# Kernel optimization log

Hardware: AMD Instinct MI355X
Metric: run time of the kernel (lower is better)

The kernel has to match this reference:

```python
import jax, jax.numpy as jnp
import numpy as np

N_NODES, IN_DIM, HID, N_CLS, N_T = 4096, 512, 256, 128, 20


def _odefunc(x, A, Wt, bt):
    # X' = relu(Linear(A @ X)); dropout=0.0 so it is the identity
    return jax.nn.relu((A @ x) @ Wt.T + bt)


def _rk4_traj(vt, x0, A, Wt, bt):
    # torchdiffeq 'rk4' = fixed-grid 3/8-rule RK4 stepping between consecutive vt points
    f = lambda y: _odefunc(y, A, Wt, bt)  # autonomous: t unused by ODEFunc

    def step(x, dt):
        k1 = f(x)
        k2 = f(x + dt * k1 / 3.0)
        k3 = f(x + dt * (k2 - k1 / 3.0))
        k4 = f(x + dt * (k1 - k2 + k3))
        xn = x + dt * (k1 + 3.0 * k2 + 3.0 * k3 + k4) / 8.0
        return xn, xn

    dts = vt[1:] - vt[:-1]
    _, ys = jax.lax.scan(step, x0, dts)
    return jnp.concatenate([x0[None], ys], axis=0)  # [T, N, H]


def setup_inputs() -> dict:
    key = jax.random.key(0)
    ks = jax.random.split(key, 8)
    vt = jnp.arange(N_T, dtype=jnp.float32) * 0.05  # increasing time ticks, horizon ~1.0
    x = jax.random.normal(ks[0], (N_NODES, IN_DIM), dtype=jnp.float32)
    # row-scaled dense adjacency (torch.mm dense path); spectral scale ~O(1)
    A = jax.random.uniform(ks[1], (N_NODES, N_NODES), dtype=jnp.float32) / N_NODES
    W1 = jax.random.normal(ks[2], (HID, IN_DIM), dtype=jnp.float32) / np.sqrt(IN_DIM)
    b1 = jnp.zeros((HID,), dtype=jnp.float32)
    W2 = jax.random.normal(ks[3], (HID, HID), dtype=jnp.float32) / np.sqrt(HID)
    b2 = jnp.zeros((HID,), dtype=jnp.float32)
    Wt = jax.random.normal(ks[4], (HID, HID), dtype=jnp.float32) * (0.5 / np.sqrt(HID))
    bt = jnp.zeros((HID,), dtype=jnp.float32)
    Wo = jax.random.normal(ks[5], (N_CLS, HID), dtype=jnp.float32) / np.sqrt(HID)
    bo = jnp.zeros((N_CLS,), dtype=jnp.float32)
    return {"vt": vt, "x": x, "A": A, "W1": W1, "b1": b1, "W2": W2,
            "b2": b2, "Wt": Wt, "bt": bt, "Wo": Wo, "bo": bo}


def reference(vt, x, A, W1, b1, W2, b2, Wt, bt, Wo, bo):
    # input_layer: Linear -> Tanh -> Linear (dropout = 0.0 elsewhere)
    h = jnp.tanh(x @ W1.T + b1) @ W2.T + b2            # [N, H]
    traj = _rk4_traj(vt, h, A, Wt, bt)                 # [T, N, H] (terminal=False -> full trajectory)
    return traj @ Wo.T + bo                            # [T, N, C]
```

## Files before the change

### kernel.cpp

```cpp
#include <hip/hip_runtime.h>
#include <stdint.h>

typedef __bf16 bf16;
typedef bf16 bf16x8 __attribute__((ext_vector_type(8)));
typedef float f32x4 __attribute__((ext_vector_type(4)));
typedef uint32_t u32;
typedef unsigned long long u64;
typedef unsigned char u8;

#define NN   4096
#define HID  256
#define NCLS 128

__device__ __forceinline__ void gload16(const void* g, void* l) {
  __builtin_amdgcn_global_load_lds((const __attribute__((address_space(1))) u32*)g,
                                   (__attribute__((address_space(3))) u32*)l, 16, 0, 0);
}

__global__ void convf2b(const float* __restrict__ s, bf16* __restrict__ d, int n) {
  int i = (blockIdx.x * blockDim.x + threadIdx.x) * 4;
  if (i >= n) return;
  f32x4 v = *(const f32x4*)(s + i);
  bf16 o[4] = {(bf16)v[0], (bf16)v[1], (bf16)v[2], (bf16)v[3]};
  *(u64*)(d + i) = *(u64*)o;
}

__global__ void convAf8(const float* __restrict__ s, u8* __restrict__ d, int n) {
  int i = (blockIdx.x * blockDim.x + threadIdx.x) * 4;
  if (i >= n) return;
  f32x4 v = *(const f32x4*)(s + i);
  u32 pk = __builtin_amdgcn_cvt_pk_fp8_f32(v[0] * 4096.f, v[1] * 4096.f, 0, false);
  pk = __builtin_amdgcn_cvt_pk_fp8_f32(v[2] * 4096.f, v[3] * 4096.f, pk, true);
  *(u32*)(d + i) = pk;
}

__device__ __forceinline__ f32x4 ksplit_reduce(char* smem, f32x4 acc[2][2],
                                               int kw, int sw, int hh, int rl) {
  float* fs = (float*)smem;
  #pragma unroll
  for (int q = 0; q < 4; ++q) {
    const int src = (kw < q) ? kw : kw - 1;
    float* dst = fs + ((q * 3 + src) * 2 + sw) * 272;
    const int mf = q >> 1, nf = q & 1;
    if (q != kw) {
      #pragma unroll
      for (int j = 0; j < 4; ++j) dst[(hh * 4 + j) * 17 + rl] = acc[mf][nf][j];
    }
  }
  asm volatile("s_waitcnt lgkmcnt(0)" ::: "memory");
  __builtin_amdgcn_s_barrier();
  f32x4 r;
  if (kw == 0)      r = acc[0][0];
  else if (kw == 1) r = acc[0][1];
  else if (kw == 2) r = acc[1][0];
  else              r = acc[1][1];
  #pragma unroll
  for (int src = 0; src < 3; ++src) {
    const float* sp = fs + ((kw * 3 + src) * 2 + sw) * 272;
    #pragma unroll
    for (int j = 0; j < 4; ++j) r[j] += sp[(hh * 4 + j) * 17 + rl];
  }
  return r;
}

__global__ __launch_bounds__(512, 2) void gemmf8(
    const u8* __restrict__ Ag,
    const u8* __restrict__ Bg,
    bf16* __restrict__ Cb)
{
  __shared__ __align__(16) char smem[73728];
  const int tid = threadIdx.x;
  const int l = tid & 63, wv = tid >> 6;
  const int kw = wv & 3, sw = wv >> 2;
  const int rl = l & 15, hh = l >> 4;

  const int chunk = gridDim.x >> 3;
  const int sb = (blockIdx.x & 7) * chunk + (blockIdx.x >> 3);
  const int m0 = (sb >> 3) * 64, n0 = (sb & 7) * 32;

  const bool isB = wv >= 4;
  const int w4 = wv & 3;
  const int rlo = l >> 4;
  const int gq = l & 15;
  const int rowbase = isB ? n0 + w4 * 8 : m0 + w4 * 16;
  const u8* sGbase = (isB ? Bg : Ag) + (size_t)rowbase * 4096;
  const int c0 = (gq ^ rlo) << 4;
  const int c1 = (gq ^ (rlo + 4)) << 4;
  const int stoff = isB ? 16384 + w4 * 2048 : w4 * 4096;

  f32x4 acc[2][2];
  #pragma unroll
  for (int i = 0; i < 2; ++i)
    #pragma unroll
    for (int j = 0; j < 2; ++j) acc[i][j] = (f32x4){0.f, 0.f, 0.f, 0.f};

  auto stage = [&](int buf, int t) {
    char* base = smem + buf * 24576 + stoff;
    const u8* g = sGbase + (size_t)rlo * 4096 + t * 256;
    gload16(g + c0,                      base);
    gload16(g + (size_t)4  * 4096 + c1,  base + 1024);
    if (!isB) {
      gload16(g + (size_t)8  * 4096 + c0, base + 2048);
      gload16(g + (size_t)12 * 4096 + c1, base + 3072);
    }
  };

  auto compute = [&](int buf) {
    const char* As = smem + buf * 24576;
    const char* Bs = As + 16384;
    #pragma unroll
    for (int ks = 0; ks < 2; ++ks) {
      const int g0 = (kw * 2 + ks) * 2 + (hh >> 1);
      const int co = ((g0 ^ (rl & 7)) << 4) + (hh & 1) * 8;
      u64 a0 = *(const u64*)(As + (sw * 32 + rl +  0) * 256 + co);
      u64 a1 = *(const u64*)(As + (sw * 32 + rl + 16) * 256 + co);
      u64 b0 = *(const u64*)(Bs + (rl +  0) * 256 + co);
      u64 b1 = *(const u64*)(Bs + (rl + 16) * 256 + co);
      __builtin_amdgcn_s_setprio(1);
      acc[0][0] = __builtin_amdgcn_mfma_f32_16x16x32_fp8_fp8((long)a0, (long)b0, acc[0][0], 0, 0, 0);
      acc[0][1] = __builtin_amdgcn_mfma_f32_16x16x32_fp8_fp8((long)a0, (long)b1, acc[0][1], 0, 0, 0);
      acc[1][0] = __builtin_amdgcn_mfma_f32_16x16x32_fp8_fp8((long)a1, (long)b0, acc[1][0], 0, 0, 0);
      acc[1][1] = __builtin_amdgcn_mfma_f32_16x16x32_fp8_fp8((long)a1, (long)b1, acc[1][1], 0, 0, 0);
      __builtin_amdgcn_s_setprio(0);
    }
  };

  stage(0, 0); stage(1, 1);
  int cur = 0, pre = 2;
  for (int t = 0; t < 16; ++t) {
    if (t < 15) {
      if (!isB) { asm volatile("s_waitcnt vmcnt(4)" ::: "memory"); }
      else      { asm volatile("s_waitcnt vmcnt(2)" ::: "memory"); }
    } else       { asm volatile("s_waitcnt vmcnt(0)" ::: "memory"); }
    __builtin_amdgcn_sched_barrier(0);
    __builtin_amdgcn_s_barrier();
    __builtin_amdgcn_sched_barrier(0);
    if (t + 2 < 16) stage(pre, t + 2);
    compute(cur);
    cur = (cur == 2) ? 0 : cur + 1;
    pre = (pre == 2) ? 0 : pre + 1;
  }
  __builtin_amdgcn_s_barrier();
  __builtin_amdgcn_sched_barrier(0);

  f32x4 o = ksplit_reduce(smem, acc, kw, sw, hh, rl);
  const int row0 = m0 + sw * 32 + (kw >> 1) * 16 + hh * 4;
  const int col  = n0 + (kw & 1) * 16 + rl;
  #pragma unroll
  for (int r = 0; r < 4; ++r)
    Cb[(row0 + r) * HID + col] = (bf16)(o[r] * 2.44140625e-4f);
}

template<int EPI, int KK>
__global__ __launch_bounds__(512, 2) void gemmbf(
    const bf16* __restrict__ Ag, int lda,
    const bf16* __restrict__ Bg, int ldb,
    int Ntiles,
    const float* __restrict__ bias,
    float* __restrict__ outf,
    bf16* __restrict__ outb,
    u8* __restrict__ ybt,
    float* __restrict__ xbuf,
    const float* __restrict__ kk1,
    const float* __restrict__ kk2,
    const float* __restrict__ kk3,
    const float* __restrict__ vt, int step)
{
  __shared__ __align__(16) char smem[49152];
  const int tid = threadIdx.x;
  const int l = tid & 63, wv = tid >> 6;
  const int kw = wv & 3, sw = wv >> 2;
  const int rl = l & 15, hh = l >> 4;

  const int chunk = gridDim.x >> 3;
  const int sb = (blockIdx.x & 7) * chunk + (blockIdx.x >> 3);
  const int mtile = sb / Ntiles;
  const int ntile = sb - mtile * Ntiles;
  const int m0 = mtile * 64, n0 = ntile * 32;

  const bool isB = wv >= 4;
  const int w4 = wv & 3;

  f32x4 acc[2][2];
  #pragma unroll
  for (int i = 0; i < 2; ++i)
    #pragma unroll
    for (int j = 0; j < 2; ++j) acc[i][j] = (f32x4){0.f, 0.f, 0.f, 0.f};

  if constexpr (KK == 256) {
    const int lrow = l >> 5, lg = l & 31;
    if (!isB) {
      const char* gb = (const char*)(Ag + (size_t)(m0 + w4 * 16) * lda);
      char* base = smem + w4 * 8192;
      #pragma unroll
      for (int i = 0; i < 8; ++i) {
        const int r = i * 2 + lrow;
        const int swz = (lg ^ ((w4 * 16 + r) & 7)) << 4;
        gload16(gb + (size_t)r * lda * 2 + swz, base + i * 1024);
      }
    } else {
      const char* gb = (const char*)(Bg + (size_t)(n0 + w4 * 8) * ldb);
      char* base = smem + 32768 + w4 * 4096;
      #pragma unroll
      for (int i = 0; i < 4; ++i) {
        const int r = i * 2 + lrow;
        const int swz = (lg ^ ((w4 * 8 + r) & 7)) << 4;
        gload16(gb + (size_t)r * ldb * 2 + swz, base + i * 1024);
      }
    }
    asm volatile("s_waitcnt vmcnt(0)" ::: "memory");
    __builtin_amdgcn_sched_barrier(0);
    __builtin_amdgcn_s_barrier();
    __builtin_amdgcn_sched_barrier(0);

    const char* As = smem;
    const char* Bs = smem + 32768;
    #pragma unroll
    for (int ks = 0; ks < 2; ++ks) {
      const int ca = ((((kw * 2 + ks) * 4 + hh) ^ (rl & 7)) << 4);
      bf16x8 a0 = *(const bf16x8*)(As + (sw * 32 + rl +  0) * 512 + ca);
      bf16x8 a1 = *(const bf16x8*)(As + (sw * 32 + rl + 16) * 512 + ca);
      bf16x8 b0 = *(const bf16x8*)(Bs + (rl +  0) * 512 + ca);
      bf16x8 b1 = *(const bf16x8*)(Bs + (rl + 16) * 512 + ca);
      __builtin_amdgcn_s_setprio(1);
      acc[0][0] = __builtin_amdgcn_mfma_f32_16x16x32_bf16(a0, b0, acc[0][0], 0, 0, 0);
      acc[0][1] = __builtin_amdgcn_mfma_f32_16x16x32_bf16(a0, b1, acc[0][1], 0, 0, 0);
      acc[1][0] = __builtin_amdgcn_mfma_f32_16x16x32_bf16(a1, b0, acc[1][0], 0, 0, 0);
      acc[1][1] = __builtin_amdgcn_mfma_f32_16x16x32_bf16(a1, b1, acc[1][1], 0, 0, 0);
      __builtin_amdgcn_s_setprio(0);
    }
    __builtin_amdgcn_s_barrier();
    __builtin_amdgcn_sched_barrier(0);
  } else {
    const int rlo = l >> 4, gq = l & 15;
    const size_t ldby = (size_t)(isB ? ldb : lda) * 2;
    const int grow = (isB ? n0 + w4 * 8 : m0 + w4 * 16) + rlo;
    const char* sGb = (const char*)(isB ? (const void*)Bg : (const void*)Ag)
                      + (size_t)grow * ldby;
    const int c0 = (gq ^ rlo) << 4;
    const int c1 = (gq ^ (rlo + 4)) << 4;
    const int stoff = isB ? 16384 + w4 * 2048 : w4 * 4096;

    auto stage = [&](int buf, int t) {
      char* base = smem + buf * 24576 + stoff;
      const char* g = sGb + (size_t)t * 256;
      gload16(g + c0,            base);
      gload16(g + 4 * ldby + c1, base + 1024);
      if (!isB) {
        gload16(g +  8 * ldby + c0, base + 2048);
        gload16(g + 12 * ldby + c1, base + 3072);
      }
    };

    const int ca = ((kw * 4 + hh) ^ (rl & 7)) << 4;
    auto compute = [&](int buf) {
      const char* As = smem + buf * 24576;
      const char* Bs = As + 16384;
      bf16x8 a0 = *(const bf16x8*)(As + (sw * 32 + rl +  0) * 256 + ca);
      bf16x8 a1 = *(const bf16x8*)(As + (sw * 32 + rl + 16) * 256 + ca);
      bf16x8 b0 = *(const bf16x8*)(Bs + (rl +  0) * 256 + ca);
      bf16x8 b1 = *(const bf16x8*)(Bs + (rl + 16) * 256 + ca);
      __builtin_amdgcn_s_setprio(1);
      acc[0][0] = __builtin_amdgcn_mfma_f32_16x16x32_bf16(a0, b0, acc[0][0], 0, 0, 0);
      acc[0][1] = __builtin_amdgcn_mfma_f32_16x16x32_bf16(a0, b1, acc[0][1], 0, 0, 0);
      acc[1][0] = __builtin_amdgcn_mfma_f32_16x16x32_bf16(a1, b0, acc[1][0], 0, 0, 0);
      acc[1][1] = __builtin_amdgcn_mfma_f32_16x16x32_bf16(a1, b1, acc[1][1], 0, 0, 0);
      __builtin_amdgcn_s_setprio(0);
    };

    const int nmac = KK >> 7;
    stage(0, 0);
    asm volatile("s_waitcnt vmcnt(0)" ::: "memory");
    __builtin_amdgcn_s_barrier();
    int cur = 0;
    for (int t = 0; t < nmac; ++t) {
      if (t + 1 < nmac) stage(cur ^ 1, t + 1);
      compute(cur);
      asm volatile("s_waitcnt vmcnt(0)" ::: "memory");
      __builtin_amdgcn_sched_barrier(0);
      __builtin_amdgcn_s_barrier();
      cur ^= 1;
    }
    __builtin_amdgcn_sched_barrier(0);
  }

  f32x4 o = ksplit_reduce(smem, acc, kw, sw, hh, rl);
  const int row0 = m0 + sw * 32 + (kw >> 1) * 16 + hh * 4;
  const int col  = n0 + (kw & 1) * 16 + rl;

  float dtv = 0.f;
  if constexpr (EPI >= 3 && EPI <= 6) dtv = vt[step + 1] - vt[step];

  if constexpr (EPI == 1) {
    #pragma unroll
    for (int r = 0; r < 4; ++r)
      outb[(row0 + r) * HID + col] = (bf16)tanhf(o[r] + bias[col]);
  } else if constexpr (EPI == 2) {
    float yv[4];
    #pragma unroll
    for (int r = 0; r < 4; ++r) {
      float v = o[r] + bias[col];
      xbuf[(row0 + r) * HID + col] = v;
      outb[(row0 + r) * HID + col] = (bf16)v;
      yv[r] = v;
    }
    u32 pk = __builtin_amdgcn_cvt_pk_fp8_f32(yv[0], yv[1], 0, false);
    pk = __builtin_amdgcn_cvt_pk_fp8_f32(yv[2], yv[3], pk, true);
    *(u32*)(ybt + (size_t)col * NN + row0) = pk;
  } else if constexpr (EPI >= 3 && EPI <= 6) {
    float yv[4];
    #pragma unroll
    for (int r = 0; r < 4; ++r) {
      const int idx = (row0 + r) * HID + col;
      float v = fmaxf(o[r] + bias[col], 0.f);
      float xv = xbuf[idx];
      float y;
      if constexpr (EPI == 3)      { outf[idx] = v; y = xv + dtv * (1.f/3.f) * v; }
      else if constexpr (EPI == 4) { outf[idx] = v; y = xv + dtv * (v - kk1[idx] * (1.f/3.f)); }
      else if constexpr (EPI == 5) { outf[idx] = v; y = xv + dtv * (kk1[idx] - kk2[idx] + v); }
      else {
        float xn = xv + dtv * 0.125f * (kk1[idx] + 3.f*kk2[idx] + 3.f*kk3[idx] + v);
        xbuf[idx] = xn;
        outb[idx] = (bf16)xn;
        y = xn;
      }
      yv[r] = y;
    }
    u32 pk = __builtin_amdgcn_cvt_pk_fp8_f32(yv[0], yv[1], 0, false);
    pk = __builtin_amdgcn_cvt_pk_fp8_f32(yv[2], yv[3], pk, true);
    *(u32*)(ybt + (size_t)col * NN + row0) = pk;
  } else {
    #pragma unroll
    for (int r = 0; r < 4; ++r)
      outf[(size_t)(row0 + r) * NCLS + col] = o[r] + bias[col];
  }
}

extern "C" void kernel_launch(void* const* d_in, const int* in_sizes, int n_in,
                              void* d_out, int out_size, void* d_ws, size_t ws_size,
                              hipStream_t stream)
{
  const float* vt = (const float*)d_in[0];
  const float* x  = (const float*)d_in[1];
  const float* A  = (const float*)d_in[2];
  const float* W1 = (const float*)d_in[3];
  const float* b1 = (const float*)d_in[4];
  const float* W2 = (const float*)d_in[5];
  const float* b2 = (const float*)d_in[6];
  const float* Wt = (const float*)d_in[7];
  const float* bt = (const float*)d_in[8];
  const float* Wo = (const float*)d_in[9];
  const float* bo = (const float*)d_in[10];
  float* out = (float*)d_out;

  char* p = (char*)d_ws;
  auto carve = [&](size_t n) { char* r = p; p += (n + 255) & ~(size_t)255; return r; };
  u8*   A8  = (u8*)carve((size_t)4096 * 4096);
  bf16* xb  = (bf16*)carve((size_t)4096 * 512 * 2);
  bf16* W1b = (bf16*)carve((size_t)256 * 512 * 2);
  bf16* W2b = (bf16*)carve((size_t)256 * 256 * 2);
  bf16* Wtb = (bf16*)carve((size_t)256 * 256 * 2);
  bf16* Wob = (bf16*)carve((size_t)128 * 256 * 2);
  bf16* T1b = (bf16*)carve((size_t)4096 * 256 * 2);
  bf16* Cb  = (bf16*)carve((size_t)4096 * 256 * 2);
  u8*   Y8  = (u8*)carve((size_t)256 * 4096);
  float* xs = (float*)carve((size_t)4096 * 256 * 4);
  float* k1 = (float*)carve((size_t)4096 * 256 * 4);
  float* k2 = (float*)carve((size_t)4096 * 256 * 4);
  float* k3 = (float*)carve((size_t)4096 * 256 * 4);
  size_t base_need = (size_t)(p - (char*)d_ws);
  const size_t trajBytes = (size_t)20 * 4096 * 256 * 2;
  bool big = (ws_size >= base_need + trajBytes);
  bf16* traj = (bf16*)carve(big ? trajBytes : (size_t)4096 * 256 * 2);

  convAf8<<<16384, 256, 0, stream>>>(A,  A8,  16777216);
  convf2b<<<2048,  256, 0, stream>>>(x,  xb,  2097152);
  convf2b<<<128,   256, 0, stream>>>(W1, W1b, 131072);
  convf2b<<<64,    256, 0, stream>>>(W2, W2b, 65536);
  convf2b<<<64,    256, 0, stream>>>(Wt, Wtb, 65536);
  convf2b<<<32,    256, 0, stream>>>(Wo, Wob, 32768);

  gemmbf<1, 512><<<512, 512, 0, stream>>>(xb, 512, W1b, 512, 8, b1,
      nullptr, T1b, nullptr, nullptr, nullptr, nullptr, nullptr, vt, 0);
  gemmbf<2, 256><<<512, 512, 0, stream>>>(T1b, 256, W2b, 256, 8, b2,
      nullptr, traj, Y8, xs, nullptr, nullptr, nullptr, vt, 0);
  if (!big)
    gemmbf<7, 256><<<256, 512, 0, stream>>>(traj, 256, Wob, 256, 4, bo,
        out, nullptr, nullptr, nullptr, nullptr, nullptr, nullptr, vt, 0);

  for (int t = 0; t < 19; ++t) {
    bf16* slot = big ? (traj + (size_t)(t + 1) * 4096 * 256) : traj;
    gemmf8<<<512, 512, 0, stream>>>(A8, Y8, Cb);
    gemmbf<3, 256><<<512, 512, 0, stream>>>(Cb, 256, Wtb, 256, 8, bt,
        k1, nullptr, Y8, xs, nullptr, nullptr, nullptr, vt, t);
    gemmf8<<<512, 512, 0, stream>>>(A8, Y8, Cb);
    gemmbf<4, 256><<<512, 512, 0, stream>>>(Cb, 256, Wtb, 256, 8, bt,
        k2, nullptr, Y8, xs, k1, nullptr, nullptr, vt, t);
    gemmf8<<<512, 512, 0, stream>>>(A8, Y8, Cb);
    gemmbf<5, 256><<<512, 512, 0, stream>>>(Cb, 256, Wtb, 256, 8, bt,
        k3, nullptr, Y8, xs, k1, k2, nullptr, vt, t);
    gemmf8<<<512, 512, 0, stream>>>(A8, Y8, Cb);
    gemmbf<6, 256><<<512, 512, 0, stream>>>(Cb, 256, Wtb, 256, 8, bt,
        nullptr, slot, Y8, xs, k1, k2, k3, vt, t);
    if (!big)
      gemmbf<7, 256><<<256, 512, 0, stream>>>(traj, 256, Wob, 256, 4, bo,
          out + (size_t)(t + 1) * 4096 * 128, nullptr, nullptr, nullptr,
          nullptr, nullptr, nullptr, vt, 0);
  }
  if (big)
    gemmbf<7, 256><<<5120, 512, 0, stream>>>(traj, 256, Wob, 256, 4, bo,
        out, nullptr, nullptr, nullptr, nullptr, nullptr, nullptr, vt, 0);
}
```

Measured before the change: 1.434 ms.

## Load fp8 A operand directly into registers, staging only B through LDS

```diff
diff --git a/kernel.cpp b/kernel.cpp
--- a/kernel.cpp
+++ b/kernel.cpp
@@ -68,7 +68,7 @@
     const u8* __restrict__ Bg,
     bf16* __restrict__ Cb)
 {
-  __shared__ __align__(16) char smem[73728];
+  __shared__ __align__(16) char smem[28672];
   const int tid = threadIdx.x;
   const int l = tid & 63, wv = tid >> 6;
   const int kw = wv & 3, sw = wv >> 2;
@@ -78,15 +78,12 @@
   const int sb = (blockIdx.x & 7) * chunk + (blockIdx.x >> 3);
   const int m0 = (sb >> 3) * 64, n0 = (sb & 7) * 32;
 
-  const bool isB = wv >= 4;
-  const int w4 = wv & 3;
-  const int rlo = l >> 4;
-  const int gq = l & 15;
-  const int rowbase = isB ? n0 + w4 * 8 : m0 + w4 * 16;
-  const u8* sGbase = (isB ? Bg : Ag) + (size_t)rowbase * 4096;
-  const int c0 = (gq ^ rlo) << 4;
-  const int c1 = (gq ^ (rlo + 4)) << 4;
-  const int stoff = isB ? 16384 + w4 * 2048 : w4 * 4096;
+  const int rlo = l >> 4, gq = l & 15;
+  const int brow = wv * 4 + rlo;
+  const u8* srcB = Bg + (size_t)(n0 + brow) * 4096 + ((gq ^ (brow & 7)) << 4);
+
+  const u8* pa0 = Ag + (size_t)(m0 + sw * 32 + rl) * 4096 + kw * 64 + hh * 8;
+  const u8* pa1 = pa0 + (size_t)16 * 4096;
 
   f32x4 acc[2][2];
   #pragma unroll
@@ -94,28 +91,42 @@
     #pragma unroll
     for (int j = 0; j < 2; ++j) acc[i][j] = (f32x4){0.f, 0.f, 0.f, 0.f};
 
-  auto stage = [&](int buf, int t) {
-    char* base = smem + buf * 24576 + stoff;
-    const u8* g = sGbase + (size_t)rlo * 4096 + t * 256;
-    gload16(g + c0,                      base);
-    gload16(g + (size_t)4  * 4096 + c1,  base + 1024);
-    if (!isB) {
-      gload16(g + (size_t)8  * 4096 + c0, base + 2048);
-      gload16(g + (size_t)12 * 4096 + c1, base + 3072);
-    }
-  };
-
-  auto compute = [&](int buf) {
-    const char* As = smem + buf * 24576;
-    const char* Bs = As + 16384;
+  u64 Ar[2][4];
+
+  Ar[0][0] = *(const u64*)(pa0);
+  Ar[0][1] = *(const u64*)(pa0 + 32);
+  Ar[0][2] = *(const u64*)(pa1);
+  Ar[0][3] = *(const u64*)(pa1 + 32);
+  gload16(srcB,       smem + wv * 1024);
+  gload16(srcB + 256, smem + 8192 + wv * 1024);
+
+  #pragma unroll
+  for (int t = 0; t < 16; ++t) {
+    if (t < 15) { asm volatile("s_waitcnt vmcnt(1)" ::: "memory"); }
+    else        { asm volatile("s_waitcnt vmcnt(0)" ::: "memory"); }
+    __builtin_amdgcn_sched_barrier(0);
+    __builtin_amdgcn_s_barrier();
+    __builtin_amdgcn_sched_barrier(0);
+    if (t + 1 < 16) {
+      const u8* qa0 = pa0 + (t + 1) * 256;
+      const u8* qa1 = pa1 + (t + 1) * 256;
+      Ar[(t + 1) & 1][0] = *(const u64*)(qa0);
+      Ar[(t + 1) & 1][1] = *(const u64*)(qa0 + 32);
+      Ar[(t + 1) & 1][2] = *(const u64*)(qa1);
+      Ar[(t + 1) & 1][3] = *(const u64*)(qa1 + 32);
+    }
+    if (t + 2 < 16)
+      gload16(srcB + (t + 2) * 256, smem + ((t + 2) % 3) * 8192 + wv * 1024);
+
+    const char* Bs = smem + (t % 3) * 8192;
     #pragma unroll
     for (int ks = 0; ks < 2; ++ks) {
-      const int g0 = (kw * 2 + ks) * 2 + (hh >> 1);
+      const int g0 = kw * 4 + ks * 2 + (hh >> 1);
       const int co = ((g0 ^ (rl & 7)) << 4) + (hh & 1) * 8;
-      u64 a0 = *(const u64*)(As + (sw * 32 + rl +  0) * 256 + co);
-      u64 a1 = *(const u64*)(As + (sw * 32 + rl + 16) * 256 + co);
       u64 b0 = *(const u64*)(Bs + (rl +  0) * 256 + co);
       u64 b1 = *(const u64*)(Bs + (rl + 16) * 256 + co);
+      const u64 a0 = Ar[t & 1][ks];
+      const u64 a1 = Ar[t & 1][2 + ks];
       __builtin_amdgcn_s_setprio(1);
       acc[0][0] = __builtin_amdgcn_mfma_f32_16x16x32_fp8_fp8((long)a0, (long)b0, acc[0][0], 0, 0, 0);
       acc[0][1] = __builtin_amdgcn_mfma_f32_16x16x32_fp8_fp8((long)a0, (long)b1, acc[0][1], 0, 0, 0);
@@ -123,22 +134,6 @@
       acc[1][1] = __builtin_amdgcn_mfma_f32_16x16x32_fp8_fp8((long)a1, (long)b1, acc[1][1], 0, 0, 0);
       __builtin_amdgcn_s_setprio(0);
     }
-  };
-
-  stage(0, 0); stage(1, 1);
-  int cur = 0, pre = 2;
-  for (int t = 0; t < 16; ++t) {
-    if (t < 15) {
-      if (!isB) { asm volatile("s_waitcnt vmcnt(4)" ::: "memory"); }
-      else      { asm volatile("s_waitcnt vmcnt(2)" ::: "memory"); }
-    } else       { asm volatile("s_waitcnt vmcnt(0)" ::: "memory"); }
-    __builtin_amdgcn_sched_barrier(0);
-    __builtin_amdgcn_s_barrier();
-    __builtin_amdgcn_sched_barrier(0);
-    if (t + 2 < 16) stage(pre, t + 2);
-    compute(cur);
-    cur = (cur == 2) ? 0 : cur + 1;
-    pre = (pre == 2) ? 0 : pre + 1;
   }
   __builtin_amdgcn_s_barrier();
   __builtin_amdgcn_sched_barrier(0);
```

New measurement: 3.001 ms. 109% more time.
